# Performance work log

Measured on AMD Instinct MI355X. Metric: run time of the kernel, lower is better.

Reference implementation:

```python
import jax, jax.numpy as jnp
import numpy as np

EPS = 1e-5  # torch InstanceNorm2d default eps


def _patches(x):
    """3x3 patches with padding 1. [B,C,H,W] -> [B,C,9,H,W]."""
    B, C, H, W = x.shape
    xp = jnp.pad(x, ((0, 0), (0, 0), (1, 1), (1, 1)))
    cols = [xp[:, :, dy:dy + H, dx:dx + W] for dy in range(3) for dx in range(3)]
    return jnp.stack(cols, axis=2)


def _instance_norm(x):
    # per-(batch, channel) normalization over spatial dims, biased variance, no affine
    mu = jnp.mean(x, axis=(2, 3), keepdims=True)
    var = jnp.mean((x - mu) ** 2, axis=(2, 3), keepdims=True)
    return (x - mu) * jax.lax.rsqrt(var + EPS)


def setup_inputs() -> dict:
    key = jax.random.key(0)
    ks = jax.random.split(key, 6)
    B, Cin, Cout, H, W = 4, 128, 64, 128, 128
    feat = jax.random.normal(ks[0], (B, Cin, H, W), dtype=jnp.float32)
    guide = jax.random.normal(ks[1], (B, Cin, H, W), dtype=jnp.float32)
    # PacConv2d weight/bias (Cin -> Cin, 3x3)
    pac_w = jax.random.normal(ks[2], (Cin, Cin, 3, 3), dtype=jnp.float32) * 0.02
    pac_b = jax.random.normal(ks[3], (Cin,), dtype=jnp.float32) * 0.02
    # decoding Conv2d weight/bias (Cin -> Cout, 3x3)
    conv_w = jax.random.normal(ks[4], (Cout, Cin, 3, 3), dtype=jnp.float32) * 0.02
    conv_b = jax.random.normal(ks[5], (Cout,), dtype=jnp.float32) * 0.02
    return {"feat": feat, "guide": guide, "pac_w": pac_w, "pac_b": pac_b,
            "conv_w": conv_w, "conv_b": conv_b}


def reference(feat, guide, pac_w, pac_b, conv_w, conv_b):
    B, C, H, W = feat.shape
    O = pac_w.shape[0]
    # --- PacConv2d: pixel-adaptive Gaussian kernel from the guide ---
    g = _patches(guide)                                   # [B,Cg,9,H,W]
    diff2 = jnp.sum((g - guide[:, :, None]) ** 2, axis=1, keepdims=True)
    kern = jnp.exp(-0.5 * diff2)                          # [B,1,9,H,W]
    f = _patches(feat) * kern                             # [B,C,9,H,W]
    pac = jnp.einsum('bckhw,ock->bohw', f, pac_w.reshape(O, C, 9))
    pac = pac + pac_b[None, :, None, None]
    # --- InstanceNorm + ReLU ---
    x = jax.nn.relu(_instance_norm(pac))
    # --- decoding: Conv2d 3x3 + InstanceNorm + ReLU ---
    y = jax.lax.conv_general_dilated(x, conv_w, window_strides=(1, 1),
                                     padding=((1, 1), (1, 1)))
    y = y + conv_b[None, :, None, None]
    return jax.nn.relu(_instance_norm(y))
```

## Files before the change

### kernel.cpp

```cpp
#include <hip/hip_runtime.h>

#define H 128
#define W 128
#define HW 16384
#define CIN 128
#define COUT 64
#define BATCH 4
#define EPS 1e-5f
#define PY 130
#define PX 132

#define FB_OFF    0
#define XNB_OFF   4392960
#define KPART_OFF XNB_OFF
#define KERN_OFF  (XNB_OFF + 4392960)
#define WT_OFF    (KERN_OFF + 589824)
#define CT_OFF    (WT_OFF + 73728)
#define STATS_OFF (CT_OFF + 36864)
#define SUM1   (STATS_OFF)
#define SUMSQ1 (STATS_OFF + 512)
#define SUM2   (STATS_OFF + 1024)
#define SUMSQ2 (STATS_OFF + 1280)
#define SCALE1 (STATS_OFF + 1536)
#define SHIFT1 (STATS_OFF + 2048)
#define SCALE2 (STATS_OFF + 2560)
#define SHIFT2 (STATS_OFF + 2816)

typedef float f32x4 __attribute__((ext_vector_type(4)));
typedef short bf16x8 __attribute__((ext_vector_type(8)));
typedef short bf16x4 __attribute__((ext_vector_type(4)));
#define MFMA16 __builtin_amdgcn_mfma_f32_16x16x32_bf16

__device__ __forceinline__ unsigned short f2b(float f) {
  union { float f; unsigned u; } un; un.f = f;
  unsigned r = un.u + 0x7FFF + ((un.u >> 16) & 1);
  return (unsigned short)(r >> 16);
}
__device__ __forceinline__ float b2f(unsigned short u) {
  union { unsigned u; float f; } x; x.u = ((unsigned)u) << 16; return x.f;
}
__device__ __forceinline__ void load_lds16(const void* g, void* l) {
  __builtin_amdgcn_global_load_lds(
      (const __attribute__((address_space(1))) unsigned int*)g,
      (__attribute__((address_space(3))) unsigned int*)l, 16, 0, 0);
}

__device__ __forceinline__ void decode_wg(int bid, int& b, int& y, int& x0) {
  int wgid = (bid & 7) * 128 + (bid >> 3);
  b = wgid >> 8;
  int rem = wgid & 255;
  y = rem >> 1;
  x0 = (rem & 1) << 6;
}

__global__ __launch_bounds__(256) void zero_pads(float* __restrict__ ws, int buf) {
  int id = blockIdx.x * 256 + threadIdx.x;
  if (id >= 4 * 776 * 16) return;
  int chunk = id & 15; int rest = id >> 4;
  int px = rest % 776; int b = rest / 776;
  int row, xx;
  if (px < 264) { row = (px < 132) ? 0 : 129; xx = px % 132; }
  else { int q = px - 264; row = 1 + (q >> 2); int m = q & 3; xx = m ? 128 + m : 0; }
  unsigned short* base = (unsigned short*)(ws + (buf ? XNB_OFF : FB_OFF));
  bf16x8 z = {0, 0, 0, 0, 0, 0, 0, 0};
  *(bf16x8*)(base + ((b * PY + row) * PX + xx) * 128 + chunk * 8) = z;
}

__global__ __launch_bounds__(256) void transpose_feat(const float* __restrict__ feat,
                                                      float* __restrict__ ws) {
  __shared__ __align__(16) char T[128 * 256];
  int b = blockIdx.x >> 7, y = blockIdx.x & 127;
  int t = threadIdx.x;
  int x = t & 127, ch = t >> 7;
  const float* fp = feat + ((b * CIN) << 14) + (y << 7) + x;
#pragma unroll 8
  for (int cc = 0; cc < 64; ++cc) {
    int c = ch * 64 + cc;
    float v = fp[c << 14];
    int byte = (x << 8) + (c << 1);
    byte ^= (x & 7) << 4;
    *(unsigned short*)(T + byte) = f2b(v);
  }
  __syncthreads();
  unsigned short* fb = (unsigned short*)(ws + FB_OFF);
#pragma unroll
  for (int it = 0; it < 8; ++it) {
    int flat = it * 256 + t;
    int px = flat >> 4, j = flat & 15;
    int byte = (px << 8) + (j << 4);
    byte ^= (px & 7) << 4;
    bf16x8 v = *(bf16x8*)(T + byte);
    *(bf16x8*)(fb + ((b * PY + y + 1) * PX + px + 1) * 128 + j * 8) = v;
  }
}

__global__ __launch_bounds__(256) void kern_part(const float* __restrict__ guide,
                                                 float* __restrict__ ws) {
  int p = blockIdx.x * 256 + threadIdx.x;
  int cs = blockIdx.y;
  int b = p >> 14;
  int pix = p & (HW - 1);
  int y = pix >> 7, x = pix & (W - 1);
  float acc[9];
#pragma unroll
  for (int k = 0; k < 9; ++k) acc[k] = 0.f;
  const float* gb = guide + ((b * CIN + cs * 32) << 14);
  for (int c = 0; c < 32; ++c) {
    const float* gc = gb + (c << 14);
    float g0 = gc[pix];
#pragma unroll
    for (int dy = -1; dy <= 1; ++dy) {
#pragma unroll
      for (int dx = -1; dx <= 1; ++dx) {
        int yy = y + dy, xx = x + dx;
        bool ok = ((unsigned)yy < (unsigned)H) && ((unsigned)xx < (unsigned)W);
        int yc = min(max(yy, 0), H - 1);
        int xc = min(max(xx, 0), W - 1);
        float g = gc[yc * W + xc];
        g = ok ? g : 0.f;
        float d = g - g0;
        acc[(dy + 1) * 3 + (dx + 1)] += d * d;
      }
    }
  }
  float* kp = ws + KPART_OFF;
#pragma unroll
  for (int k = 0; k < 9; ++k)
    kp[(((cs * BATCH + b) * 9 + k) << 14) + pix] = acc[k];
}

__global__ __launch_bounds__(256) void expk(float* __restrict__ ws) {
  int i = blockIdx.x * 256 + threadIdx.x;
  const float4* kp = reinterpret_cast<const float4*>(ws + KPART_OFF);
  float4 a = kp[i], b = kp[i + 147456], c = kp[i + 2 * 147456], d = kp[i + 3 * 147456];
  float4 o;
  o.x = __expf(-0.5f * (a.x + b.x + c.x + d.x));
  o.y = __expf(-0.5f * (a.y + b.y + c.y + d.y));
  o.z = __expf(-0.5f * (a.z + b.z + c.z + d.z));
  o.w = __expf(-0.5f * (a.w + b.w + c.w + d.w));
  reinterpret_cast<float4*>(ws + KERN_OFF)[i] = o;
}

__global__ __launch_bounds__(256) void prep_w(const float* __restrict__ pw,
                                              const float* __restrict__ cw,
                                              float* __restrict__ ws) {
  int t = blockIdx.x * 256 + threadIdx.x;
  unsigned short* Wtu = (unsigned short*)(ws + WT_OFF);
  unsigned short* Ctu = (unsigned short*)(ws + CT_OFF);
  if (t < 147456) {
    int k = t >> 14, rem = t & 16383, o = rem >> 7, c = rem & 127;
    Wtu[t] = f2b(pw[(o * CIN + c) * 9 + k]);
  } else {
    int u = t - 147456;
    int k = u >> 13, rem = u & 8191, o = rem >> 7, c = rem & 127;
    Ctu[u] = f2b(cw[(o * CIN + c) * 9 + k]);
  }
}

__device__ __forceinline__ void stage_tile(const unsigned short* __restrict__ src_base,
                                           char* Fs, int b, int y, int x0, int t) {
  int lane = t & 63, w = t >> 6;
  int j = lane & 15, pl = lane >> 4;
#pragma unroll
  for (int q = 0; q < 12; ++q) {
    int m = w * 12 + q;
    int r = m >> 4, pblk = m & 15;
    int p = 1 + pblk * 4 + pl;
    int jx = (j & 8) | ((j & 7) ^ (p & 7));
    const unsigned short* src = src_base + (((b * PY + y + r) * PX + x0 + p) << 7) + jx * 8;
    char* dst = Fs + ((r * 66 + 1 + pblk * 4) << 8);
    load_lds16(src, dst);
  }
  if (t < 96) {
    int r = t >> 5, side = (t >> 4) & 1, jj = t & 15;
    int p = side ? 65 : 0;
    int jx = (jj & 8) | ((jj & 7) ^ (p & 7));
    const unsigned short* src = src_base + (((b * PY + y + r) * PX + x0 + p) << 7) + jx * 8;
    bf16x8 v = *(const bf16x8*)src;
    *(bf16x8*)(Fs + ((r * 66 + p) << 8) + jj * 16) = v;
  }
}

__global__ __launch_bounds__(256, 2) void pac_mfma(float* __restrict__ ws) {
  __shared__ __align__(16) char Fs[3 * 66 * 256];
  int b, y, x0;
  decode_wg(blockIdx.x, b, y, x0);
  const int t = threadIdx.x;
  const unsigned short* Wtu = (const unsigned short*)(ws + WT_OFF);
  const unsigned short* fb = (const unsigned short*)(ws + FB_OFF);
  unsigned short* xnb = (unsigned short*)(ws + XNB_OFF);
  const int lane = t & 63, l15 = lane & 15, lg = lane >> 4;
  const int o0 = (t >> 6) * 32;

  const unsigned short* Wbase = Wtu + (o0 + l15) * 128 + lg * 8;
  const float* kernb = ws + KERN_OFF + ((b * 9) << 14) + (y << 7) + x0 + l15;

  bf16x8 wa[3][8];
  float kr[3][4];
#pragma unroll
  for (int pk = 0; pk < 2; ++pk) {
#pragma unroll
    for (int ks = 0; ks < 4; ++ks) {
      wa[pk][ks * 2 + 0] = *(const bf16x8*)(Wbase + pk * 16384 + ks * 32);
      wa[pk][ks * 2 + 1] = *(const bf16x8*)(Wbase + pk * 16384 + 2048 + ks * 32);
    }
#pragma unroll
    for (int pt = 0; pt < 4; ++pt) kr[pk][pt] = kernb[(pk << 14) + pt * 16];
  }

  stage_tile(fb, Fs, b, y, x0, t);
  __syncthreads();

  const f32x4 vzero = {0.f, 0.f, 0.f, 0.f};
  f32x4 pacc0[4], pacc1[4];
#pragma unroll
  for (int pt = 0; pt < 4; ++pt) { pacc0[pt] = vzero; pacc1[pt] = vzero; }

#pragma unroll
  for (int k = 0; k < 9; ++k) {
    const int dy = k / 3, dxi = k % 3;
    const int cur = k % 3;
    if (k + 2 <= 8) {
      const int nb = (k + 2) % 3;
#pragma unroll
      for (int ks = 0; ks < 4; ++ks) {
        wa[nb][ks * 2 + 0] = *(const bf16x8*)(Wbase + (k + 2) * 16384 + ks * 32);
        wa[nb][ks * 2 + 1] = *(const bf16x8*)(Wbase + (k + 2) * 16384 + 2048 + ks * 32);
      }
#pragma unroll
      for (int pt = 0; pt < 4; ++pt) kr[nb][pt] = kernb[((k + 2) << 14) + pt * 16];
    }
    f32x4 z0[4], z1[4];
#pragma unroll
    for (int ks = 0; ks < 4; ++ks) {
#pragma unroll
      for (int pt = 0; pt < 4; ++pt) {
        int p = dxi + pt * 16 + l15;
        int byte = ((dy * 66 + p) << 8) + ks * 64 + lg * 16;
        byte ^= (p & 7) << 4;
        bf16x8 bv = *(const bf16x8*)(Fs + byte);
        z0[pt] = MFMA16(wa[cur][ks * 2 + 0], bv, ks ? z0[pt] : vzero, 0, 0, 0);
        z1[pt] = MFMA16(wa[cur][ks * 2 + 1], bv, ks ? z1[pt] : vzero, 0, 0, 0);
      }
    }
#pragma unroll
    for (int pt = 0; pt < 4; ++pt) {
      float kvv = kr[cur][pt];
#pragma unroll
      for (int i = 0; i < 4; ++i) {
        pacc0[pt][i] = fmaf(kvv, z0[pt][i], pacc0[pt][i]);
        pacc1[pt][i] = fmaf(kvv, z1[pt][i], pacc1[pt][i]);
      }
    }
  }

  float* sum1 = ws + SUM1;
  float* sumsq1 = ws + SUMSQ1;
#pragma unroll
  for (int pt = 0; pt < 4; ++pt) {
    int px = x0 + pt * 16 + l15;
    int base = ((b * PY + y + 1) * PX + px + 1) * 128;
    bf16x4 vA, vB;
#pragma unroll
    for (int i = 0; i < 4; ++i) { vA[i] = (short)f2b(pacc0[pt][i]); vB[i] = (short)f2b(pacc1[pt][i]); }
    *(bf16x4*)(xnb + base + o0 + lg * 4) = vA;
    *(bf16x4*)(xnb + base + o0 + 16 + lg * 4) = vB;
  }
#pragma unroll
  for (int half = 0; half < 2; ++half) {
#pragma unroll
    for (int i = 0; i < 4; ++i) {
      float s = 0.f, sq = 0.f;
#pragma unroll
      for (int pt = 0; pt < 4; ++pt) {
        float v = half ? pacc1[pt][i] : pacc0[pt][i];
        s += v; sq += v * v;
      }
#pragma unroll
      for (int m = 1; m < 16; m <<= 1) {
        s += __shfl_xor(s, m);
        sq += __shfl_xor(sq, m);
      }
      if (l15 == 0) {
        int o = o0 + half * 16 + lg * 4 + i;
        atomicAdd(&sum1[b * CIN + o], s);
        atomicAdd(&sumsq1[b * CIN + o], sq);
      }
    }
  }
}

__global__ void stats_kernel(float* __restrict__ ws, int sumoff, int sqoff,
                             int scoff, int shoff, int n, float invN) {
  int i = blockIdx.x * blockDim.x + threadIdx.x;
  if (i >= n) return;
  float mu = ws[sumoff + i] * invN;
  float var = ws[sqoff + i] * invN - mu * mu;
  var = fmaxf(var, 0.f);
  float rs = rsqrtf(var + EPS);
  ws[scoff + i] = rs;
  ws[shoff + i] = -mu * rs;
}

__global__ __launch_bounds__(256) void nrm(float* __restrict__ ws) {
  int b = blockIdx.x >> 7, y = blockIdx.x & 127;
  unsigned short* xnb = (unsigned short*)(ws + XNB_OFF);
  const float* sc = ws + SCALE1 + b * CIN;
  const float* sh = ws + SHIFT1 + b * CIN;
  int t = threadIdx.x;
  int rowbase = ((b * PY + y + 1) * PX + 1) * 128;
#pragma unroll
  for (int it = 0; it < 8; ++it) {
    int flat = it * 256 + t;
    int px = flat >> 4, j = flat & 15;
    unsigned short* p = xnb + rowbase + px * 128 + j * 8;
    bf16x8 v = *(bf16x8*)p;
    f32x4 s0 = *(const f32x4*)(sc + j * 8), s1 = *(const f32x4*)(sc + j * 8 + 4);
    f32x4 h0 = *(const f32x4*)(sh + j * 8), h1 = *(const f32x4*)(sh + j * 8 + 4);
    bf16x8 o;
#pragma unroll
    for (int e = 0; e < 4; ++e) {
      o[e] = (short)f2b(fmaxf(fmaf(b2f((unsigned short)v[e]), s0[e], h0[e]), 0.f));
      o[e + 4] = (short)f2b(fmaxf(fmaf(b2f((unsigned short)v[e + 4]), s1[e], h1[e]), 0.f));
    }
    *(bf16x8*)p = o;
  }
}

__global__ __launch_bounds__(256, 3) void conv_mfma(float* __restrict__ ws,
                                                    float* __restrict__ out) {
  __shared__ __align__(16) char Xs[3 * 66 * 256];
  int b, y, x0;
  decode_wg(blockIdx.x, b, y, x0);
  const int t = threadIdx.x;
  const unsigned short* Ctu = (const unsigned short*)(ws + CT_OFF);
  const unsigned short* xnb = (const unsigned short*)(ws + XNB_OFF);
  const int lane = t & 63, l15 = lane & 15, lg = lane >> 4;
  const int o0 = (t >> 6) * 16;

  const unsigned short* Cbase = Ctu + (o0 + l15) * 128 + lg * 8;

  bf16x8 wa[3][4];
#pragma unroll
  for (int pk = 0; pk < 2; ++pk)
#pragma unroll
    for (int ks = 0; ks < 4; ++ks)
      wa[pk][ks] = *(const bf16x8*)(Cbase + pk * 8192 + ks * 32);

  stage_tile(xnb, Xs, b, y, x0, t);
  __syncthreads();

  const f32x4 vzero = {0.f, 0.f, 0.f, 0.f};
  f32x4 acc[4];
#pragma unroll
  for (int pt = 0; pt < 4; ++pt) acc[pt] = vzero;

#pragma unroll
  for (int k = 0; k < 9; ++k) {
    const int dy = k / 3, dxi = k % 3;
    const int cur = k % 3;
    if (k + 2 <= 8) {
      const int nb = (k + 2) % 3;
#pragma unroll
      for (int ks = 0; ks < 4; ++ks)
        wa[nb][ks] = *(const bf16x8*)(Cbase + (k + 2) * 8192 + ks * 32);
    }
#pragma unroll
    for (int ks = 0; ks < 4; ++ks) {
#pragma unroll
      for (int pt = 0; pt < 4; ++pt) {
        int p = dxi + pt * 16 + l15;
        int byte = ((dy * 66 + p) << 8) + ks * 64 + lg * 16;
        byte ^= (p & 7) << 4;
        bf16x8 bv = *(const bf16x8*)(Xs + byte);
        acc[pt] = MFMA16(wa[cur][ks], bv, acc[pt], 0, 0, 0);
      }
    }
  }

  float* sum2 = ws + SUM2;
  float* sumsq2 = ws + SUMSQ2;
#pragma unroll
  for (int pt = 0; pt < 4; ++pt) {
#pragma unroll
    for (int i = 0; i < 4; ++i) {
      int o = o0 + lg * 4 + i;
      int px = x0 + pt * 16 + l15;
      out[((b * COUT + o) << 14) + (y << 7) + px] = acc[pt][i];
    }
  }
#pragma unroll
  for (int i = 0; i < 4; ++i) {
    float s = 0.f, sq = 0.f;
#pragma unroll
    for (int pt = 0; pt < 4; ++pt) { float v = acc[pt][i]; s += v; sq += v * v; }
#pragma unroll
    for (int m = 1; m < 16; m <<= 1) {
      s += __shfl_xor(s, m);
      sq += __shfl_xor(sq, m);
    }
    if (l15 == 0) {
      int o = o0 + lg * 4 + i;
      atomicAdd(&sum2[b * COUT + o], s);
      atomicAdd(&sumsq2[b * COUT + o], sq);
    }
  }
}

__global__ __launch_bounds__(256) void norm_kernel(float* __restrict__ out,
                                                   const float* __restrict__ ws) {
  int i = blockIdx.x * 256 + threadIdx.x;
  int bc = (i * 4) >> 14;
  float sc = ws[SCALE2 + bc];
  float sh = ws[SHIFT2 + bc];
  float4 v = reinterpret_cast<float4*>(out)[i];
  v.x = fmaxf(fmaf(v.x, sc, sh), 0.f);
  v.y = fmaxf(fmaf(v.y, sc, sh), 0.f);
  v.z = fmaxf(fmaf(v.z, sc, sh), 0.f);
  v.w = fmaxf(fmaf(v.w, sc, sh), 0.f);
  reinterpret_cast<float4*>(out)[i] = v;
}

extern "C" void kernel_launch(void* const* d_in, const int* in_sizes, int n_in,
                              void* d_out, int out_size, void* d_ws, size_t ws_size,
                              hipStream_t stream) {
  const float* feat = (const float*)d_in[0];
  const float* guide = (const float*)d_in[1];
  const float* pac_w = (const float*)d_in[2];
  const float* conv_w = (const float*)d_in[4];
  float* ws = (float*)d_ws;
  float* out = (float*)d_out;

  hipMemsetAsync(ws + STATS_OFF, 0, 1536 * sizeof(float), stream);

  prep_w<<<dim3(864), 256, 0, stream>>>(pac_w, conv_w, ws);
  zero_pads<<<dim3(194), 256, 0, stream>>>(ws, 0);
  transpose_feat<<<dim3(512), 256, 0, stream>>>(feat, ws);
  kern_part<<<dim3(256, 4), 256, 0, stream>>>(guide, ws);
  expk<<<dim3(576), 256, 0, stream>>>(ws);
  zero_pads<<<dim3(194), 256, 0, stream>>>(ws, 1);
  pac_mfma<<<dim3(1024), 256, 0, stream>>>(ws);
  stats_kernel<<<dim3(2), 256, 0, stream>>>(ws, SUM1, SUMSQ1, SCALE1, SHIFT1,
                                            BATCH * CIN, 1.f / HW);
  nrm<<<dim3(512), 256, 0, stream>>>(ws);
  conv_mfma<<<dim3(1024), 256, 0, stream>>>(ws, out);
  stats_kernel<<<dim3(1), 256, 0, stream>>>(ws, SUM2, SUMSQ2, SCALE2, SHIFT2,
                                            BATCH * COUT, 1.f / HW);
  norm_kernel<<<dim3(BATCH * COUT * HW / 1024), 256, 0, stream>>>(out, ws);
}
```

Baseline: 167.0 us.

## Compute two output rows per workgroup in PAC and decoding convolutions

Each workgroup in pac_mfma and conv_mfma now covers two adjacent output rows instead of one. It stages a 4-row halo tile in LDS instead of 3 rows and reuses each weight-fragment load across both rows. The grids shrink from 1024 to 512 workgroups, which cuts weight traffic per output and halo redundancy, and halves the stat atomics. The cost is more accumulator registers, larger LDS use, conv_mfma's occupancy hint dropping from 3 to 2, and fewer workgroups to fill the 256 CUs.

```diff
diff --git a/kernel.cpp b/kernel.cpp
--- a/kernel.cpp
+++ b/kernel.cpp
@@ -45,11 +45,11 @@
       (__attribute__((address_space(3))) unsigned int*)l, 16, 0, 0);
 }
 
-__device__ __forceinline__ void decode_wg(int bid, int& b, int& y, int& x0) {
-  int wgid = (bid & 7) * 128 + (bid >> 3);
-  b = wgid >> 8;
-  int rem = wgid & 255;
-  y = rem >> 1;
+__device__ __forceinline__ void decode_wg2(int bid, int& b, int& y, int& x0) {
+  int wgid = (bid & 7) * 64 + (bid >> 3);
+  b = wgid >> 7;
+  int rem = wgid & 127;
+  y = (rem >> 1) << 1;
   x0 = (rem & 1) << 6;
 }
 
@@ -157,21 +157,20 @@
   }
 }
 
-__device__ __forceinline__ void stage_tile(const unsigned short* __restrict__ src_base,
-                                           char* Fs, int b, int y, int x0, int t) {
+__device__ __forceinline__ void stage_tile4(const unsigned short* __restrict__ src_base,
+                                            char* Fs, int b, int y, int x0, int t) {
   int lane = t & 63, w = t >> 6;
   int j = lane & 15, pl = lane >> 4;
 #pragma unroll
-  for (int q = 0; q < 12; ++q) {
-    int m = w * 12 + q;
-    int r = m >> 4, pblk = m & 15;
+  for (int q = 0; q < 16; ++q) {
+    int r = w, pblk = q;
     int p = 1 + pblk * 4 + pl;
     int jx = (j & 8) | ((j & 7) ^ (p & 7));
     const unsigned short* src = src_base + (((b * PY + y + r) * PX + x0 + p) << 7) + jx * 8;
     char* dst = Fs + ((r * 66 + 1 + pblk * 4) << 8);
     load_lds16(src, dst);
   }
-  if (t < 96) {
+  if (t < 128) {
     int r = t >> 5, side = (t >> 4) & 1, jj = t & 15;
     int p = side ? 65 : 0;
     int jx = (jj & 8) | ((jj & 7) ^ (p & 7));
@@ -182,9 +181,9 @@
 }
 
 __global__ __launch_bounds__(256, 2) void pac_mfma(float* __restrict__ ws) {
-  __shared__ __align__(16) char Fs[3 * 66 * 256];
+  __shared__ __align__(16) char Fs[4 * 66 * 256];
   int b, y, x0;
-  decode_wg(blockIdx.x, b, y, x0);
+  decode_wg2(blockIdx.x, b, y, x0);
   const int t = threadIdx.x;
   const unsigned short* Wtu = (const unsigned short*)(ws + WT_OFF);
   const unsigned short* fb = (const unsigned short*)(ws + FB_OFF);
@@ -193,28 +192,31 @@
   const int o0 = (t >> 6) * 32;
 
   const unsigned short* Wbase = Wtu + (o0 + l15) * 128 + lg * 8;
-  const float* kernb = ws + KERN_OFF + ((b * 9) << 14) + (y << 7) + x0 + l15;
+  const float* kernb0 = ws + KERN_OFF + ((b * 9) << 14) + (y << 7) + x0 + l15;
 
   bf16x8 wa[3][8];
-  float kr[3][4];
-#pragma unroll
-  for (int pk = 0; pk < 2; ++pk) {
+  float kr[2][2][4];
+#pragma unroll
+  for (int pk = 0; pk < 2; ++pk)
 #pragma unroll
     for (int ks = 0; ks < 4; ++ks) {
       wa[pk][ks * 2 + 0] = *(const bf16x8*)(Wbase + pk * 16384 + ks * 32);
       wa[pk][ks * 2 + 1] = *(const bf16x8*)(Wbase + pk * 16384 + 2048 + ks * 32);
     }
 #pragma unroll
-    for (int pt = 0; pt < 4; ++pt) kr[pk][pt] = kernb[(pk << 14) + pt * 16];
-  }
-
-  stage_tile(fb, Fs, b, y, x0, t);
+  for (int yr = 0; yr < 2; ++yr)
+#pragma unroll
+    for (int pt = 0; pt < 4; ++pt) kr[0][yr][pt] = kernb0[(yr << 7) + pt * 16];
+
+  stage_tile4(fb, Fs, b, y, x0, t);
   __syncthreads();
 
   const f32x4 vzero = {0.f, 0.f, 0.f, 0.f};
-  f32x4 pacc0[4], pacc1[4];
-#pragma unroll
-  for (int pt = 0; pt < 4; ++pt) { pacc0[pt] = vzero; pacc1[pt] = vzero; }
+  f32x4 pacc0[2][4], pacc1[2][4];
+#pragma unroll
+  for (int yr = 0; yr < 2; ++yr)
+#pragma unroll
+    for (int pt = 0; pt < 4; ++pt) { pacc0[yr][pt] = vzero; pacc1[yr][pt] = vzero; }
 
 #pragma unroll
   for (int k = 0; k < 9; ++k) {
@@ -227,29 +229,38 @@
         wa[nb][ks * 2 + 0] = *(const bf16x8*)(Wbase + (k + 2) * 16384 + ks * 32);
         wa[nb][ks * 2 + 1] = *(const bf16x8*)(Wbase + (k + 2) * 16384 + 2048 + ks * 32);
       }
-#pragma unroll
-      for (int pt = 0; pt < 4; ++pt) kr[nb][pt] = kernb[((k + 2) << 14) + pt * 16];
-    }
-    f32x4 z0[4], z1[4];
-#pragma unroll
-    for (int ks = 0; ks < 4; ++ks) {
+    }
+    if (k + 1 <= 8) {
+#pragma unroll
+      for (int yr = 0; yr < 2; ++yr)
+#pragma unroll
+        for (int pt = 0; pt < 4; ++pt)
+          kr[(k + 1) & 1][yr][pt] = kernb0[((k + 1) << 14) + (yr << 7) + pt * 16];
+    }
+#pragma unroll
+    for (int yr = 0; yr < 2; ++yr) {
+      const int rr = dy + yr;
+      f32x4 z0[4], z1[4];
+#pragma unroll
+      for (int ks = 0; ks < 4; ++ks) {
+#pragma unroll
+        for (int pt = 0; pt < 4; ++pt) {
+          int p = dxi + pt * 16 + l15;
+          int byte = ((rr * 66 + p) << 8) + ks * 64 + lg * 16;
+          byte ^= (p & 7) << 4;
+          bf16x8 bv = *(const bf16x8*)(Fs + byte);
+          z0[pt] = MFMA16(wa[cur][ks * 2 + 0], bv, ks ? z0[pt] : vzero, 0, 0, 0);
+          z1[pt] = MFMA16(wa[cur][ks * 2 + 1], bv, ks ? z1[pt] : vzero, 0, 0, 0);
+        }
+      }
 #pragma unroll
       for (int pt = 0; pt < 4; ++pt) {
-        int p = dxi + pt * 16 + l15;
-        int byte = ((dy * 66 + p) << 8) + ks * 64 + lg * 16;
-        byte ^= (p & 7) << 4;
-        bf16x8 bv = *(const bf16x8*)(Fs + byte);
-        z0[pt] = MFMA16(wa[cur][ks * 2 + 0], bv, ks ? z0[pt] : vzero, 0, 0, 0);
-        z1[pt] = MFMA16(wa[cur][ks * 2 + 1], bv, ks ? z1[pt] : vzero, 0, 0, 0);
-      }
-    }
-#pragma unroll
-    for (int pt = 0; pt < 4; ++pt) {
-      float kvv = kr[cur][pt];
-#pragma unroll
-      for (int i = 0; i < 4; ++i) {
-        pacc0[pt][i] = fmaf(kvv, z0[pt][i], pacc0[pt][i]);
-        pacc1[pt][i] = fmaf(kvv, z1[pt][i], pacc1[pt][i]);
+        float kvv = kr[k & 1][yr][pt];
+#pragma unroll
+        for (int i = 0; i < 4; ++i) {
+          pacc0[yr][pt][i] = fmaf(kvv, z0[pt][i], pacc0[yr][pt][i]);
+          pacc1[yr][pt][i] = fmaf(kvv, z1[pt][i], pacc1[yr][pt][i]);
+        }
       }
     }
   }
@@ -257,25 +268,32 @@
   float* sum1 = ws + SUM1;
   float* sumsq1 = ws + SUMSQ1;
 #pragma unroll
-  for (int pt = 0; pt < 4; ++pt) {
-    int px = x0 + pt * 16 + l15;
-    int base = ((b * PY + y + 1) * PX + px + 1) * 128;
-    bf16x4 vA, vB;
-#pragma unroll
-    for (int i = 0; i < 4; ++i) { vA[i] = (short)f2b(pacc0[pt][i]); vB[i] = (short)f2b(pacc1[pt][i]); }
-    *(bf16x4*)(xnb + base + o0 + lg * 4) = vA;
-    *(bf16x4*)(xnb + base + o0 + 16 + lg * 4) = vB;
-  }
+  for (int yr = 0; yr < 2; ++yr)
+#pragma unroll
+    for (int pt = 0; pt < 4; ++pt) {
+      int px = x0 + pt * 16 + l15;
+      int base = ((b * PY + y + yr + 1) * PX + px + 1) * 128;
+      bf16x4 vA, vB;
+#pragma unroll
+      for (int i = 0; i < 4; ++i) {
+        vA[i] = (short)f2b(pacc0[yr][pt][i]);
+        vB[i] = (short)f2b(pacc1[yr][pt][i]);
+      }
+      *(bf16x4*)(xnb + base + o0 + lg * 4) = vA;
+      *(bf16x4*)(xnb + base + o0 + 16 + lg * 4) = vB;
+    }
 #pragma unroll
   for (int half = 0; half < 2; ++half) {
 #pragma unroll
     for (int i = 0; i < 4; ++i) {
       float s = 0.f, sq = 0.f;
 #pragma unroll
-      for (int pt = 0; pt < 4; ++pt) {
-        float v = half ? pacc1[pt][i] : pacc0[pt][i];
-        s += v; sq += v * v;
-      }
+      for (int yr = 0; yr < 2; ++yr)
+#pragma unroll
+        for (int pt = 0; pt < 4; ++pt) {
+          float v = half ? pacc1[yr][pt][i] : pacc0[yr][pt][i];
+          s += v; sq += v * v;
+        }
 #pragma unroll
       for (int m = 1; m < 16; m <<= 1) {
         s += __shfl_xor(s, m);
@@ -327,11 +345,11 @@
   }
 }
 
-__global__ __launch_bounds__(256, 3) void conv_mfma(float* __restrict__ ws,
+__global__ __launch_bounds__(256, 2) void conv_mfma(float* __restrict__ ws,
                                                     float* __restrict__ out) {
-  __shared__ __align__(16) char Xs[3 * 66 * 256];
+  __shared__ __align__(16) char Xs[4 * 66 * 256];
   int b, y, x0;
-  decode_wg(blockIdx.x, b, y, x0);
+  decode_wg2(blockIdx.x, b, y, x0);
   const int t = threadIdx.x;
   const unsigned short* Ctu = (const unsigned short*)(ws + CT_OFF);
   const unsigned short* xnb = (const unsigned short*)(ws + XNB_OFF);
@@ -347,13 +365,15 @@
     for (int ks = 0; ks < 4; ++ks)
       wa[pk][ks] = *(const bf16x8*)(Cbase + pk * 8192 + ks * 32);
 
-  stage_tile(xnb, Xs, b, y, x0, t);
+  stage_tile4(xnb, Xs, b, y, x0, t);
   __syncthreads();
 
   const f32x4 vzero = {0.f, 0.f, 0.f, 0.f};
-  f32x4 acc[4];
-#pragma unroll
-  for (int pt = 0; pt < 4; ++pt) acc[pt] = vzero;
+  f32x4 acc[2][4];
+#pragma unroll
+  for (int yr = 0; yr < 2; ++yr)
+#pragma unroll
+    for (int pt = 0; pt < 4; ++pt) acc[yr][pt] = vzero;
 
 #pragma unroll
   for (int k = 0; k < 9; ++k) {
@@ -366,14 +386,18 @@
         wa[nb][ks] = *(const bf16x8*)(Cbase + (k + 2) * 8192 + ks * 32);
     }
 #pragma unroll
-    for (int ks = 0; ks < 4; ++ks) {
-#pragma unroll
-      for (int pt = 0; pt < 4; ++pt) {
-        int p = dxi + pt * 16 + l15;
-        int byte = ((dy * 66 + p) << 8) + ks * 64 + lg * 16;
-        byte ^= (p & 7) << 4;
-        bf16x8 bv = *(const bf16x8*)(Xs + byte);
-        acc[pt] = MFMA16(wa[cur][ks], bv, acc[pt], 0, 0, 0);
+    for (int yr = 0; yr < 2; ++yr) {
+      const int rr = dy + yr;
+#pragma unroll
+      for (int ks = 0; ks < 4; ++ks) {
+#pragma unroll
+        for (int pt = 0; pt < 4; ++pt) {
+          int p = dxi + pt * 16 + l15;
+          int byte = ((rr * 66 + p) << 8) + ks * 64 + lg * 16;
+          byte ^= (p & 7) << 4;
+          bf16x8 bv = *(const bf16x8*)(Xs + byte);
+          acc[yr][pt] = MFMA16(wa[cur][ks], bv, acc[yr][pt], 0, 0, 0);
+        }
       }
     }
   }
@@ -381,19 +405,23 @@
   float* sum2 = ws + SUM2;
   float* sumsq2 = ws + SUMSQ2;
 #pragma unroll
-  for (int pt = 0; pt < 4; ++pt) {
-#pragma unroll
-    for (int i = 0; i < 4; ++i) {
-      int o = o0 + lg * 4 + i;
-      int px = x0 + pt * 16 + l15;
-      out[((b * COUT + o) << 14) + (y << 7) + px] = acc[pt][i];
-    }
-  }
+  for (int yr = 0; yr < 2; ++yr)
+#pragma unroll
+    for (int pt = 0; pt < 4; ++pt) {
+#pragma unroll
+      for (int i = 0; i < 4; ++i) {
+        int o = o0 + lg * 4 + i;
+        int px = x0 + pt * 16 + l15;
+        out[((b * COUT + o) << 14) + ((y + yr) << 7) + px] = acc[yr][pt][i];
+      }
+    }
 #pragma unroll
   for (int i = 0; i < 4; ++i) {
     float s = 0.f, sq = 0.f;
 #pragma unroll
-    for (int pt = 0; pt < 4; ++pt) { float v = acc[pt][i]; s += v; sq += v * v; }
+    for (int yr = 0; yr < 2; ++yr)
+#pragma unroll
+      for (int pt = 0; pt < 4; ++pt) { float v = acc[yr][pt][i]; s += v; sq += v * v; }
 #pragma unroll
     for (int m = 1; m < 16; m <<= 1) {
       s += __shfl_xor(s, m);
@@ -439,11 +467,11 @@
   kern_part<<<dim3(256, 4), 256, 0, stream>>>(guide, ws);
   expk<<<dim3(576), 256, 0, stream>>>(ws);
   zero_pads<<<dim3(194), 256, 0, stream>>>(ws, 1);
-  pac_mfma<<<dim3(1024), 256, 0, stream>>>(ws);
+  pac_mfma<<<dim3(512), 256, 0, stream>>>(ws);
   stats_kernel<<<dim3(2), 256, 0, stream>>>(ws, SUM1, SUMSQ1, SCALE1, SHIFT1,
                                             BATCH * CIN, 1.f / HW);
   nrm<<<dim3(512), 256, 0, stream>>>(ws);
-  conv_mfma<<<dim3(1024), 256, 0, stream>>>(ws, out);
+  conv_mfma<<<dim3(512), 256, 0, stream>>>(ws, out);
   stats_kernel<<<dim3(1), 256, 0, stream>>>(ws, SUM2, SUMSQ2, SCALE2, SHIFT2,
                                             BATCH * COUT, 1.f / HW);
   norm_kernel<<<dim3(BATCH * COUT * HW / 1024), 256, 0, stream>>>(out, ws);
```

Result: slower. 235.0 us (+40.7%).
